# Kernel optimization log

Hardware: AMD Instinct MI355X
Metric: run time of the kernel (lower is better)

Reference implementation:

```python
import jax, jax.numpy as jnp
import numpy as np

N = 50000
E = 1600000
D_IN = 64
D_H = 64
D_EMB = 64
D_DEC = 128
B = 4096


def setup_inputs() -> dict:
    key = jax.random.key(0)
    ks = jax.random.split(key, 16)
    def lin(k, fan_in, fan_out):
        return jax.random.normal(k, (fan_in, fan_out), jnp.float32) / np.sqrt(fan_in)
    inp = {
        "x": jax.random.normal(ks[0], (N, D_IN), jnp.float32),
        "edge_index": jax.random.randint(ks[1], (2, E), 0, N),
        "drug_index": jax.random.randint(ks[2], (B, 2), 1, N),
        "bn_gamma": jnp.ones((D_IN,), jnp.float32),
        "bn_beta": jnp.zeros((D_IN,), jnp.float32),
        "Wu1": lin(ks[3], D_IN, D_H), "Wd1": lin(ks[4], D_IN, D_H), "Wb1": lin(ks[5], D_IN, D_H),
        "Wu2": lin(ks[6], 3 * D_H, D_H), "Wd2": lin(ks[7], 3 * D_H, D_H), "Wb2": lin(ks[8], 3 * D_H, D_H),
        "Wu3": lin(ks[9], 3 * D_H, D_EMB), "Wd3": lin(ks[10], 3 * D_H, D_EMB), "Wb3": lin(ks[11], 3 * D_H, D_EMB),
        "P1": jax.random.normal(ks[12], (3 * D_EMB, D_DEC), jnp.float32),
        "P2": jax.random.normal(ks[13], (D_DEC, D_DEC), jnp.float32),
    }
    return inp


def _batchnorm(x, gamma, beta, eps=1e-5):
    mu = jnp.mean(x, axis=0)
    var = jnp.var(x, axis=0)  # biased, matches torch BN training normalization
    return gamma * (x - mu) / jnp.sqrt(var + eps) + beta


def _bgnn_conv(x, row, col, Wu, Wd, Wb, n_nodes):
    # up direction: messages flow row -> col (source_to_target)
    up = x @ Wu
    dn = x @ Wd
    bi = x @ Wb
    ones = jnp.ones(row.shape[0], x.dtype)
    deg_up = jax.ops.segment_sum(ones, col, num_segments=n_nodes)  # in-degree at col
    x_up = jax.ops.segment_sum(up[row] / deg_up[col][:, None], col, num_segments=n_nodes)
    # down direction: flipped edge_index -> messages flow col -> row
    deg_dn = jax.ops.segment_sum(ones, row, num_segments=n_nodes)
    x_dn = jax.ops.segment_sum(dn[col] / deg_dn[row][:, None], row, num_segments=n_nodes)
    c = jnp.concatenate([x_up, x_dn, bi], axis=-1)
    nrm = jnp.linalg.norm(c, axis=-1, keepdims=True)
    return c / jnp.maximum(nrm, 1e-12)


def _leaky(t):
    return jnp.where(t >= 0, t, 0.1 * t)


def reference(x, edge_index, drug_index, bn_gamma, bn_beta,
              Wu1, Wd1, Wb1, Wu2, Wd2, Wb2, Wu3, Wd3, Wb3, P1, P2):
    row, col = edge_index[0], edge_index[1]
    h = _batchnorm(x, bn_gamma, bn_beta)
    h = _leaky(_bgnn_conv(h, row, col, Wu1, Wd1, Wb1, N))
    h = _leaky(_bgnn_conv(h, row, col, Wu2, Wd2, Wb2, N))
    h = _leaky(_bgnn_conv(h, row, col, Wu3, Wd3, Wb3, N))
    di = jnp.reshape(drug_index, (-1, 2))
    a = h[di[:, 0] - 1]  # [B, 3*D_EMB]
    b = h[di[:, 1] - 1]
    M = P1 @ P2 @ P1.T  # [3*D_EMB, 3*D_EMB]
    ypred = jnp.einsum('bd,de,be->b', a, M, b)[:, None]
    return ypred
```

## Files before the change

kernel.cpp:

```cpp
#include <hip/hip_runtime.h>

#define PN 50000
#define PE 1600000
#define PB 4096
#define NW 8
#define WSZ 6250
#define SCAP 250000
#define NSL 8

typedef __attribute__((ext_vector_type(8))) short bf16x8;
typedef __attribute__((ext_vector_type(4))) float f32x4;

__device__ inline float b2f(ushort u) {
    union { unsigned int i; float f; } x; x.i = ((unsigned int)u) << 16; return x.f;
}
__device__ inline ushort f2b(float f) {
    union { float f; unsigned int i; } x; x.f = f;
    unsigned int r = (x.i + 0x7FFFu + ((x.i >> 16) & 1u)) >> 16;
    return (ushort)r;
}

static constexpr size_t IDXCAP2 = PE + 7 * (size_t)PN + 1024;
static constexpr size_t OFF_BN     = 0;
static constexpr size_t OFF_GCUR   = 256;
static constexpr size_t OFF_TMPM   = 272;
static constexpr size_t OFF_M      = OFF_TMPM + 192 * 128;
static constexpr size_t OFF_DEGU   = OFF_M + 192 * 192;
static constexpr size_t OFF_DEGD   = OFF_DEGU + PN;
static constexpr size_t OFF_OFFU   = OFF_DEGD + PN;
static constexpr size_t OFF_OFFD   = OFF_OFFU + PN + 4;
static constexpr size_t OFF_PHISTU = OFF_OFFD + PN + 4;
static constexpr size_t OFF_PHISTD = OFF_PHISTU + NSL * (size_t)PN;
static constexpr size_t OFF_IDXU   = OFF_PHISTD + NSL * (size_t)PN;
static constexpr size_t OFF_IDXD   = OFF_IDXU + (IDXCAP2 + 1) / 2;
static constexpr size_t OFF_STGU   = OFF_IDXD + (IDXCAP2 + 1) / 2;
static constexpr size_t OFF_STGD   = OFF_STGU + 8 * (size_t)SCAP;
static constexpr size_t OFF_WB16   = OFF_STGD + 8 * (size_t)SCAP;
static constexpr size_t OFF_HB     = OFF_WB16 + 43008;
static constexpr size_t OFF_PROJ   = OFF_HB + (size_t)PN * 96;

__global__ __launch_bounds__(256) void bn_stats_kernel(const float* __restrict__ x,
                                                       float* __restrict__ sums, int N) {
    __shared__ float ls[256], ls2[256];
    int col = threadIdx.x & 63;
    int rstart = blockIdx.x * 4 + (threadIdx.x >> 6);
    float s = 0.f, s2 = 0.f;
    for (int r = rstart; r < N; r += gridDim.x * 4) {
        float v = x[(size_t)r * 64 + col];
        s += v; s2 += v * v;
    }
    ls[threadIdx.x] = s; ls2[threadIdx.x] = s2;
    __syncthreads();
    if (threadIdx.x < 64) {
        s  = ls[threadIdx.x]  + ls[threadIdx.x + 64]  + ls[threadIdx.x + 128]  + ls[threadIdx.x + 192];
        s2 = ls2[threadIdx.x] + ls2[threadIdx.x + 64] + ls2[threadIdx.x + 128] + ls2[threadIdx.x + 192];
        atomicAdd(&sums[col], s);
        atomicAdd(&sums[64 + col], s2);
    }
}

__global__ __launch_bounds__(64) void bn_finalize_kernel(const float* __restrict__ gamma,
                                                         const float* __restrict__ beta,
                                                         float* __restrict__ bn, int N) {
    int c = threadIdx.x;
    float mean = bn[c] / (float)N;
    float var = bn[64 + c] / (float)N - mean * mean;
    float sc = gamma[c] * rsqrtf(var + 1e-5f);
    bn[128 + c] = sc;
    bn[192 + c] = beta[c] - mean * sc;
}

__global__ __launch_bounds__(256) void bin_kernel(const int* __restrict__ ei,
                                                  int* __restrict__ gcur,
                                                  uint* __restrict__ stgu,
                                                  uint* __restrict__ stgd, int E) {
    __shared__ uint sbuf[16][1024];
    __shared__ int scnt[16], sbase[16];
    const int tid = threadIdx.x;
    for (int base = blockIdx.x * 1024; base < E; base += gridDim.x * 1024) {
        if (tid < 16) scnt[tid] = 0;
        __syncthreads();
#pragma unroll
        for (int j = 0; j < 4; ++j) {
            int e = base + j * 256 + tid;
            if (e < E) {
                int r = __builtin_nontemporal_load(&ei[e]);
                int c = __builtin_nontemporal_load(&ei[E + e]);
                int pu = c / WSZ;
                int slot = atomicAdd(&scnt[pu], 1);
                sbuf[pu][slot] = ((uint)c << 16) | (uint)r;
                int pd = r / WSZ;
                int slot2 = atomicAdd(&scnt[8 + pd], 1);
                sbuf[8 + pd][slot2] = ((uint)r << 16) | (uint)c;
            }
        }
        __syncthreads();
        if (tid < 16) sbase[tid] = atomicAdd(&gcur[tid], scnt[tid]);
        __syncthreads();
#pragma unroll 1
        for (int k = 0; k < 16; ++k) {
            int cnt = scnt[k];
            int gb = sbase[k];
            uint* dst = (k < 8) ? (stgu + (size_t)k * SCAP) : (stgd + (size_t)(k - 8) * SCAP);
            for (int i = tid; i < cnt; i += 256) {
                int gi = gb + i;
                if (gi < SCAP) dst[gi] = sbuf[k][i];
            }
        }
        __syncthreads();
    }
}

__global__ __launch_bounds__(256) void hist_kernel(const uint* __restrict__ stgu,
                                                   const uint* __restrict__ stgd,
                                                   const int* __restrict__ gcur,
                                                   int* __restrict__ phistu,
                                                   int* __restrict__ phistd) {
    __shared__ int hist[WSZ];
    const int p = blockIdx.x & 7;
    const int dir = (blockIdx.x >> 3) & 1;
    const int s = blockIdx.x >> 4;
    const int tid = threadIdx.x;
    const int lo = p * WSZ;
    for (int i = tid; i < WSZ; i += 256) hist[i] = 0;
    __syncthreads();
    const int cnt = min(gcur[dir * 8 + p], SCAP);
    const uint* stg = (dir ? stgd : stgu) + (size_t)p * SCAP;
    const int per = (cnt + NSL - 1) / NSL;
    const int s0 = s * per, s1 = min(cnt, s0 + per);
    for (int i = s0 + tid; i < s1; i += 256)
        atomicAdd(&hist[(int)(stg[i] >> 16) - lo], 1);
    __syncthreads();
    int* ph = (dir ? phistd : phistu) + (size_t)s * PN + lo;
    for (int i = tid; i < WSZ; i += 256) ph[i] = hist[i];
}

__global__ __launch_bounds__(1024) void scan_kernel(const int* __restrict__ phA,
                                                    const int* __restrict__ phB,
                                                    int* __restrict__ offA,
                                                    int* __restrict__ offB,
                                                    int* __restrict__ degA,
                                                    int* __restrict__ degB, int len) {
    const int* ph = blockIdx.x ? phB : phA;
    int* off = blockIdx.x ? offB : offA;
    int* dego = blockIdx.x ? degB : degA;
    __shared__ int wsum[17];
    int tid = threadIdx.x, lane = tid & 63, wid = tid >> 6;
    int run = 0;
    for (int base = 0; base < len; base += 4096) {
        int i4 = base + tid * 4;
        int4 v = make_int4(0, 0, 0, 0);
        if (i4 < len) {
#pragma unroll
            for (int sl = 0; sl < NSL; ++sl) {
                int4 t = *(const int4*)&ph[(size_t)sl * len + i4];
                v.x += t.x; v.y += t.y; v.z += t.z; v.w += t.w;
            }
            *(int4*)&dego[i4] = v;
        }
        v.x = (v.x + 7) & ~7; v.y = (v.y + 7) & ~7;
        v.z = (v.z + 7) & ~7; v.w = (v.w + 7) & ~7;
        int lsum = v.x + v.y + v.z + v.w;
        int inc = lsum;
#pragma unroll
        for (int d = 1; d < 64; d <<= 1) {
            int t = __shfl_up(inc, d);
            if (lane >= d) inc += t;
        }
        if (lane == 63) wsum[wid] = inc;
        __syncthreads();
        if (tid == 0) {
            int r2 = 0;
#pragma unroll
            for (int i = 0; i < 16; ++i) { int t = wsum[i]; wsum[i] = r2; r2 += t; }
            wsum[16] = r2;
        }
        __syncthreads();
        if (i4 < len) {
            int pre = run + wsum[wid] + inc - lsum;
            int4 o;
            o.x = pre; o.y = pre + v.x; o.z = o.y + v.y; o.w = o.z + v.z;
            *(int4*)&off[i4] = o;
        }
        run += wsum[16];
        __syncthreads();
    }
    if (tid == 0) off[len] = run;
}

__global__ __launch_bounds__(256) void scatter_kernel(const uint* __restrict__ stgu,
                                                      const uint* __restrict__ stgd,
                                                      const int* __restrict__ gcur,
                                                      const int* __restrict__ phistu,
                                                      const int* __restrict__ phistd,
                                                      const int* __restrict__ offu,
                                                      const int* __restrict__ offd,
                                                      ushort* __restrict__ idxu,
                                                      ushort* __restrict__ idxd) {
    __shared__ int cur[WSZ];
    const int p = blockIdx.x & 7;
    const int dir = (blockIdx.x >> 3) & 1;
    const int s = blockIdx.x >> 4;
    const int tid = threadIdx.x;
    const int lo = p * WSZ;
    const int* off = (dir ? offd : offu);
    const int* phist = (dir ? phistd : phistu);
    for (int i = tid; i < WSZ; i += 256) {
        int c = off[lo + i];
        for (int t = 0; t < s; ++t) c += phist[(size_t)t * PN + lo + i];
        cur[i] = c;
    }
    __syncthreads();
    const int cnt = min(gcur[dir * 8 + p], SCAP);
    const uint* stg = (dir ? stgd : stgu) + (size_t)p * SCAP;
    ushort* idx = (dir ? idxd : idxu);
    const int per = (cnt + NSL - 1) / NSL;
    const int s0 = s * per, s1 = min(cnt, s0 + per);
    for (int i = s0 + tid; i < s1; i += 256) {
        uint u = stg[i];
        int pos = atomicAdd(&cur[(int)(u >> 16) - lo], 1);
        idx[pos] = (ushort)(u & 0xFFFFu);
    }
}

template<int K>
__global__ __launch_bounds__(256) void wconv_kernel(const float* __restrict__ Wu,
                                                    const float* __restrict__ Wd,
                                                    const float* __restrict__ Wb,
                                                    ushort* __restrict__ out) {
    int idx = blockIdx.x * 256 + threadIdx.x;
    if (idx >= 192 * K) return;
    int c = idx / K, k = idx - c * K;
    const float* W = (c < 64) ? Wu : (c < 128 ? Wd : Wb);
    out[idx] = f2b(W[k * 64 + (c & 63)]);
}

template<int K, bool BN>
__global__ __launch_bounds__(256) void gemm_kernel(const ushort* __restrict__ hb,
                                                   const float* __restrict__ x,
                                                   const float* __restrict__ bn,
                                                   const ushort* __restrict__ wb,
                                                   ushort* __restrict__ proj, int nrows) {
    constexpr int KP = K + 8;
    __shared__ ushort wlds[192 * KP];
    const int tid = threadIdx.x;
    constexpr int KB8 = K / 8;
    for (int idx = tid; idx < 192 * KB8; idx += 256) {
        int col = idx / KB8, kb = idx - col * KB8;
        *(bf16x8*)&wlds[col * KP + kb * 8] = *(const bf16x8*)&wb[(size_t)col * K + kb * 8];
    }
    __syncthreads();
    const int lane = tid & 63, wid = tid >> 6;
    const int kgrp = (lane >> 4) * 8;
    const int rbase = blockIdx.x * 128 + wid * 32;
    int ar[2] = { min(rbase + (lane & 15), nrows - 1),
                  min(rbase + 16 + (lane & 15), nrows - 1) };
    f32x4 acc[2][12];
#pragma unroll
    for (int rt = 0; rt < 2; ++rt)
#pragma unroll
        for (int ct = 0; ct < 12; ++ct) acc[rt][ct] = (f32x4)0.0f;

#pragma unroll
    for (int k0 = 0; k0 < K; k0 += 32) {
        bf16x8 af[2];
        if (BN) {
#pragma unroll
            for (int rt = 0; rt < 2; ++rt)
#pragma unroll
                for (int j = 0; j < 8; ++j) {
                    int c = k0 + kgrp + j;
                    float v = x[(size_t)ar[rt] * 64 + c] * bn[128 + c] + bn[192 + c];
                    af[rt][j] = (short)f2b(v);
                }
        } else {
#pragma unroll
            for (int rt = 0; rt < 2; ++rt)
                af[rt] = *(const bf16x8*)&hb[(size_t)ar[rt] * 192 + k0 + kgrp];
        }
#pragma unroll
        for (int ct = 0; ct < 12; ++ct) {
            bf16x8 bfr = *(const bf16x8*)&wlds[(ct * 16 + (lane & 15)) * KP + k0 + kgrp];
            acc[0][ct] = __builtin_amdgcn_mfma_f32_16x16x32_bf16(af[0], bfr, acc[0][ct], 0, 0, 0);
            acc[1][ct] = __builtin_amdgcn_mfma_f32_16x16x32_bf16(af[1], bfr, acc[1][ct], 0, 0, 0);
        }
    }
    const int orow0 = blockIdx.x * 128 + wid * 32 + (lane >> 4) * 4;
#pragma unroll
    for (int rt = 0; rt < 2; ++rt)
#pragma unroll
        for (int ct = 0; ct < 12; ++ct) {
            int ocol = ct * 16 + (lane & 15);
#pragma unroll
            for (int j = 0; j < 4; ++j) {
                int orow = orow0 + rt * 16 + j;
                if (orow < nrows) proj[(size_t)orow * 192 + ocol] = f2b(acc[rt][ct][j]);
            }
        }
}

__global__ __launch_bounds__(256) void gather_kernel(const ushort* __restrict__ proj,
                                                     const int* __restrict__ offu,
                                                     const ushort* __restrict__ idxu,
                                                     const int* __restrict__ degu,
                                                     const int* __restrict__ offd,
                                                     const ushort* __restrict__ idxd,
                                                     const int* __restrict__ degd,
                                                     ushort* __restrict__ hb, int N) {
    int n = blockIdx.x * 4 + (threadIdx.x >> 6);
    if (n >= N) return;
    const int lane = threadIdx.x & 63;
    const int half = lane >> 5;
    const int sl = lane & 31;
    const int du = degu[n], dd = degd[n];
    const int d = half ? dd : du;
    const ushort* __restrict__ pidx = half ? (idxd + offd[n]) : (idxu + offu[n]);
    const uint* __restrict__ rowbase = (const uint*)proj + half * 32 + sl;
    float a0 = 0.f, a1 = 0.f;
    const int dmax = max(du, dd);
    for (int i = 0; i < dmax; i += 4) {
        ushort4 U = *(const ushort4*)(pidx + i);
        int v0 = (i     < d), v1 = (i + 1 < d), v2 = (i + 2 < d), v3 = (i + 3 < d);
        int s0 = v0 ? (int)U.x : 0;
        int s1 = v1 ? (int)U.y : 0;
        int s2 = v2 ? (int)U.z : 0;
        int s3 = v3 ? (int)U.w : 0;
        uint w0 = rowbase[(size_t)s0 * 96];
        uint w1 = rowbase[(size_t)s1 * 96];
        uint w2 = rowbase[(size_t)s2 * 96];
        uint w3 = rowbase[(size_t)s3 * 96];
        if (!v0) w0 = 0; if (!v1) w1 = 0; if (!v2) w2 = 0; if (!v3) w3 = 0;
        a0 += __uint_as_float(w0 << 16) + __uint_as_float(w1 << 16)
            + __uint_as_float(w2 << 16) + __uint_as_float(w3 << 16);
        a1 += __uint_as_float(w0 & 0xFFFF0000u) + __uint_as_float(w1 & 0xFFFF0000u)
            + __uint_as_float(w2 & 0xFFFF0000u) + __uint_as_float(w3 & 0xFFFF0000u);
    }
    float scale = 1.0f / (float)max(d, 1);
    a0 *= scale; a1 *= scale;
    uint bw = (half == 0) ? ((const uint*)proj)[(size_t)n * 96 + 64 + sl] : 0u;
    float b0 = __uint_as_float(bw << 16);
    float b1 = __uint_as_float(bw & 0xFFFF0000u);
    float ss = a0 * a0 + a1 * a1 + b0 * b0 + b1 * b1;
#pragma unroll
    for (int off = 32; off; off >>= 1) ss += __shfl_xor(ss, off);
    float r = 1.0f / fmaxf(sqrtf(ss), 1e-12f);
    a0 *= r; a1 *= r; b0 *= r; b1 *= r;
    a0 = a0 >= 0.f ? a0 : 0.1f * a0;
    a1 = a1 >= 0.f ? a1 : 0.1f * a1;
    uint* hb32 = (uint*)hb;
    hb32[(size_t)n * 96 + half * 32 + sl] = (uint)f2b(a0) | ((uint)f2b(a1) << 16);
    if (half == 0) {
        b0 = b0 >= 0.f ? b0 : 0.1f * b0;
        b1 = b1 >= 0.f ? b1 : 0.1f * b1;
        hb32[(size_t)n * 96 + 64 + sl] = (uint)f2b(b0) | ((uint)f2b(b1) << 16);
    }
}

__global__ __launch_bounds__(128) void m1_kernel(const float* __restrict__ P1,
                                                 const float* __restrict__ P2,
                                                 float* __restrict__ tmpM) {
    int i = blockIdx.x, c = threadIdx.x;
    float s = 0.f;
    for (int k = 0; k < 128; ++k) s += P1[i * 128 + k] * P2[k * 128 + c];
    tmpM[i * 128 + c] = s;
}

__global__ __launch_bounds__(192) void m2_kernel(const float* __restrict__ tmpM,
                                                 const float* __restrict__ P1,
                                                 float* __restrict__ M) {
    __shared__ float trow[128];
    int i = blockIdx.x, j = threadIdx.x;
    if (j < 128) trow[j] = tmpM[i * 128 + j];
    __syncthreads();
    float s = 0.f;
    for (int k = 0; k < 128; ++k) s += trow[k] * P1[j * 128 + k];
    M[i * 192 + j] = s;
}

__global__ __launch_bounds__(192) void decode_kernel(const ushort* __restrict__ hb,
                                                     const int* __restrict__ di,
                                                     const float* __restrict__ M,
                                                     float* __restrict__ out) {
    __shared__ alignas(16) float bvs[8][192];
    __shared__ float red[3][8];
    int pb = blockIdx.x * 8;
    int i = threadIdx.x;
#pragma unroll
    for (int p = 0; p < 8; ++p) {
        int nb = di[(pb + p) * 2 + 1] - 1;
        bvs[p][i] = b2f(hb[(size_t)nb * 192 + i]);
    }
    __syncthreads();
    float t[8] = {};
    const float4* M4 = (const float4*)(M + (size_t)i * 192);
    for (int j4 = 0; j4 < 48; ++j4) {
        float4 m = M4[j4];
#pragma unroll
        for (int p = 0; p < 8; ++p) {
            float4 b = *(const float4*)&bvs[p][j4 * 4];
            t[p] += m.x * b.x + m.y * b.y + m.z * b.z + m.w * b.w;
        }
    }
    int wid = i >> 6, lane = i & 63;
#pragma unroll
    for (int p = 0; p < 8; ++p) {
        int na = di[(pb + p) * 2] - 1;
        float v = b2f(hb[(size_t)na * 192 + i]) * t[p];
#pragma unroll
        for (int off = 32; off; off >>= 1) v += __shfl_xor(v, off);
        if (lane == 0) red[wid][p] = v;
    }
    __syncthreads();
    if (i < 8) out[pb + i] = red[0][i] + red[1][i] + red[2][i];
}

extern "C" void kernel_launch(void* const* d_in, const int* in_sizes, int n_in,
                              void* d_out, int out_size, void* d_ws, size_t ws_size,
                              hipStream_t stream) {
    const float* x     = (const float*)d_in[0];
    const int*   ei    = (const int*)d_in[1];
    const int*   di    = (const int*)d_in[2];
    const float* gamma = (const float*)d_in[3];
    const float* beta  = (const float*)d_in[4];
    const float* Wu[3] = {(const float*)d_in[5], (const float*)d_in[8],  (const float*)d_in[11]};
    const float* Wd[3] = {(const float*)d_in[6], (const float*)d_in[9],  (const float*)d_in[12]};
    const float* Wb[3] = {(const float*)d_in[7], (const float*)d_in[10], (const float*)d_in[13]};
    const float* P1    = (const float*)d_in[14];
    const float* P2    = (const float*)d_in[15];
    float* out = (float*)d_out;
    float* ws  = (float*)d_ws;

    float* bn    = ws + OFF_BN;
    int* gcur  = (int*)(ws + OFF_GCUR);
    float* tmpM  = ws + OFF_TMPM;
    float* M     = ws + OFF_M;
    int* degu  = (int*)(ws + OFF_DEGU);
    int* degd  = (int*)(ws + OFF_DEGD);
    int* offu  = (int*)(ws + OFF_OFFU);
    int* offd  = (int*)(ws + OFF_OFFD);
    int* phistu = (int*)(ws + OFF_PHISTU);
    int* phistd = (int*)(ws + OFF_PHISTD);
    ushort* idxu = (ushort*)(ws + OFF_IDXU);
    ushort* idxd = (ushort*)(ws + OFF_IDXD);
    uint* stgu = (uint*)(ws + OFF_STGU);
    uint* stgd = (uint*)(ws + OFF_STGD);
    ushort* wb16 = (ushort*)(ws + OFF_WB16);
    ushort* hb   = (ushort*)(ws + OFF_HB);
    ushort* proj = (ushort*)(ws + OFF_PROJ);
    ushort* wbl[3] = {wb16, wb16 + 12288, wb16 + 49152};

    hipMemsetAsync(ws, 0, 272 * sizeof(float), stream);

    bn_stats_kernel<<<200, 256, 0, stream>>>(x, bn, PN);
    bn_finalize_kernel<<<1, 64, 0, stream>>>(gamma, beta, bn, PN);

    bin_kernel<<<512, 256, 0, stream>>>(ei, gcur, stgu, stgd, PE);
    hist_kernel<<<16 * NSL, 256, 0, stream>>>(stgu, stgd, gcur, phistu, phistd);
    scan_kernel<<<2, 1024, 0, stream>>>(phistu, phistd, offu, offd, degu, degd, PN);
    scatter_kernel<<<16 * NSL, 256, 0, stream>>>(stgu, stgd, gcur, phistu, phistd,
                                                 offu, offd, idxu, idxd);

    wconv_kernel<64><<<(192 * 64 + 255) / 256, 256, 0, stream>>>(Wu[0], Wd[0], Wb[0], wbl[0]);
    wconv_kernel<192><<<(192 * 192 + 255) / 256, 256, 0, stream>>>(Wu[1], Wd[1], Wb[1], wbl[1]);
    wconv_kernel<192><<<(192 * 192 + 255) / 256, 256, 0, stream>>>(Wu[2], Wd[2], Wb[2], wbl[2]);

    const int ngb = (PN + 127) / 128;
    gemm_kernel<64, true><<<ngb, 256, 0, stream>>>(hb, x, bn, wbl[0], proj, PN);
    gather_kernel<<<(PN + 3) / 4, 256, 0, stream>>>(proj, offu, idxu, degu, offd, idxd, degd, hb, PN);
    gemm_kernel<192, false><<<ngb, 256, 0, stream>>>(hb, x, bn, wbl[1], proj, PN);
    gather_kernel<<<(PN + 3) / 4, 256, 0, stream>>>(proj, offu, idxu, degu, offd, idxd, degd, hb, PN);
    gemm_kernel<192, false><<<ngb, 256, 0, stream>>>(hb, x, bn, wbl[2], proj, PN);
    gather_kernel<<<(PN + 3) / 4, 256, 0, stream>>>(proj, offu, idxu, degu, offd, idxd, degd, hb, PN);

    m1_kernel<<<192, 128, 0, stream>>>(P1, P2, tmpM);
    m2_kernel<<<192, 192, 0, stream>>>(tmpM, P1, M);
    decode_kernel<<<PB / 8, 192, 0, stream>>>(hb, di, M, out);
}
```

Measured before the change: 637.1 us.

## Sub-bucket CSR edges by source window and gather window-by-window across nodes

```diff
diff --git a/kernel.cpp b/kernel.cpp
--- a/kernel.cpp
+++ b/kernel.cpp
@@ -3,10 +3,14 @@
 #define PN 50000
 #define PE 1600000
 #define PB 4096
-#define NW 8
-#define WSZ 6250
-#define SCAP 250000
-#define NSL 8
+#define NP 8
+#define PSZ 6250
+#define NSW 4
+#define SWSZ 12500
+#define SCAP 210000
+#define NSL 4
+#define GBLK 2048
+#define NPER 7
 
 typedef __attribute__((ext_vector_type(8))) short bf16x8;
 typedef __attribute__((ext_vector_type(4))) float f32x4;
@@ -20,22 +24,23 @@
     return (ushort)r;
 }
 
-static constexpr size_t IDXCAP2 = PE + 7 * (size_t)PN + 1024;
+static constexpr size_t L4N = 4 * (size_t)PN;
+static constexpr size_t IDXCAP3 = PE + 3 * L4N + 1024;
 static constexpr size_t OFF_BN     = 0;
 static constexpr size_t OFF_GCUR   = 256;
 static constexpr size_t OFF_TMPM   = 272;
 static constexpr size_t OFF_M      = OFF_TMPM + 192 * 128;
-static constexpr size_t OFF_DEGU   = OFF_M + 192 * 192;
-static constexpr size_t OFF_DEGD   = OFF_DEGU + PN;
-static constexpr size_t OFF_OFFU   = OFF_DEGD + PN;
-static constexpr size_t OFF_OFFD   = OFF_OFFU + PN + 4;
-static constexpr size_t OFF_PHISTU = OFF_OFFD + PN + 4;
-static constexpr size_t OFF_PHISTD = OFF_PHISTU + NSL * (size_t)PN;
-static constexpr size_t OFF_IDXU   = OFF_PHISTD + NSL * (size_t)PN;
-static constexpr size_t OFF_IDXD   = OFF_IDXU + (IDXCAP2 + 1) / 2;
-static constexpr size_t OFF_STGU   = OFF_IDXD + (IDXCAP2 + 1) / 2;
-static constexpr size_t OFF_STGD   = OFF_STGU + 8 * (size_t)SCAP;
-static constexpr size_t OFF_WB16   = OFF_STGD + 8 * (size_t)SCAP;
+static constexpr size_t OFF_WOFFU  = OFF_M + 192 * 192;
+static constexpr size_t OFF_WOFFD  = OFF_WOFFU + L4N + 4;
+static constexpr size_t OFF_WDEGU  = OFF_WOFFD + L4N + 4;
+static constexpr size_t OFF_WDEGD  = OFF_WDEGU + L4N;
+static constexpr size_t OFF_PHISTU = OFF_WDEGD + L4N;
+static constexpr size_t OFF_PHISTD = OFF_PHISTU + NSL * L4N;
+static constexpr size_t OFF_IDXU   = OFF_PHISTD + NSL * L4N;
+static constexpr size_t OFF_IDXD   = OFF_IDXU + (IDXCAP3 + 1) / 2;
+static constexpr size_t OFF_STGU   = OFF_IDXD + (IDXCAP3 + 1) / 2;
+static constexpr size_t OFF_STGD   = OFF_STGU + NP * (size_t)SCAP;
+static constexpr size_t OFF_WB16   = OFF_STGD + NP * (size_t)SCAP;
 static constexpr size_t OFF_HB     = OFF_WB16 + 43008;
 static constexpr size_t OFF_PROJ   = OFF_HB + (size_t)PN * 96;
 
@@ -86,10 +91,10 @@
             if (e < E) {
                 int r = __builtin_nontemporal_load(&ei[e]);
                 int c = __builtin_nontemporal_load(&ei[E + e]);
-                int pu = c / WSZ;
+                int pu = c / PSZ;
                 int slot = atomicAdd(&scnt[pu], 1);
                 sbuf[pu][slot] = ((uint)c << 16) | (uint)r;
-                int pd = r / WSZ;
+                int pd = r / PSZ;
                 int slot2 = atomicAdd(&scnt[8 + pd], 1);
                 sbuf[8 + pd][slot2] = ((uint)r << 16) | (uint)c;
             }
@@ -116,23 +121,27 @@
                                                    const int* __restrict__ gcur,
                                                    int* __restrict__ phistu,
                                                    int* __restrict__ phistd) {
-    __shared__ int hist[WSZ];
+    __shared__ int hist[PSZ * NSW];
     const int p = blockIdx.x & 7;
     const int dir = (blockIdx.x >> 3) & 1;
     const int s = blockIdx.x >> 4;
     const int tid = threadIdx.x;
-    const int lo = p * WSZ;
-    for (int i = tid; i < WSZ; i += 256) hist[i] = 0;
+    const int lo = p * PSZ;
+    for (int i = tid; i < PSZ * NSW; i += 256) hist[i] = 0;
     __syncthreads();
     const int cnt = min(gcur[dir * 8 + p], SCAP);
     const uint* stg = (dir ? stgd : stgu) + (size_t)p * SCAP;
     const int per = (cnt + NSL - 1) / NSL;
     const int s0 = s * per, s1 = min(cnt, s0 + per);
-    for (int i = s0 + tid; i < s1; i += 256)
-        atomicAdd(&hist[(int)(stg[i] >> 16) - lo], 1);
-    __syncthreads();
-    int* ph = (dir ? phistd : phistu) + (size_t)s * PN + lo;
-    for (int i = tid; i < WSZ; i += 256) ph[i] = hist[i];
+    for (int i = s0 + tid; i < s1; i += 256) {
+        uint u = stg[i];
+        int ld = (int)(u >> 16) - lo;
+        int w = (int)(u & 0xFFFFu) / SWSZ;
+        atomicAdd(&hist[ld * NSW + w], 1);
+    }
+    __syncthreads();
+    int* ph = (dir ? phistd : phistu) + (size_t)s * L4N + (size_t)lo * NSW;
+    for (int i = tid; i < PSZ * NSW; i += 256) ph[i] = hist[i];
 }
 
 __global__ __launch_bounds__(1024) void scan_kernel(const int* __restrict__ phA,
@@ -158,8 +167,8 @@
             }
             *(int4*)&dego[i4] = v;
         }
-        v.x = (v.x + 7) & ~7; v.y = (v.y + 7) & ~7;
-        v.z = (v.z + 7) & ~7; v.w = (v.w + 7) & ~7;
+        v.x = (v.x + 3) & ~3; v.y = (v.y + 3) & ~3;
+        v.z = (v.z + 3) & ~3; v.w = (v.w + 3) & ~3;
         int lsum = v.x + v.y + v.z + v.w;
         int inc = lsum;
 #pragma unroll
@@ -193,21 +202,22 @@
                                                       const int* __restrict__ gcur,
                                                       const int* __restrict__ phistu,
                                                       const int* __restrict__ phistd,
-                                                      const int* __restrict__ offu,
-                                                      const int* __restrict__ offd,
+                                                      const int* __restrict__ woffu,
+                                                      const int* __restrict__ woffd,
                                                       ushort* __restrict__ idxu,
                                                       ushort* __restrict__ idxd) {
-    __shared__ int cur[WSZ];
+    __shared__ int cur[PSZ * NSW];
     const int p = blockIdx.x & 7;
     const int dir = (blockIdx.x >> 3) & 1;
     const int s = blockIdx.x >> 4;
     const int tid = threadIdx.x;
-    const int lo = p * WSZ;
-    const int* off = (dir ? offd : offu);
+    const int lo = p * PSZ;
+    const int* off = (dir ? woffd : woffu);
     const int* phist = (dir ? phistd : phistu);
-    for (int i = tid; i < WSZ; i += 256) {
-        int c = off[lo + i];
-        for (int t = 0; t < s; ++t) c += phist[(size_t)t * PN + lo + i];
+    const size_t gb = (size_t)lo * NSW;
+    for (int i = tid; i < PSZ * NSW; i += 256) {
+        int c = off[gb + i];
+        for (int t = 0; t < s; ++t) c += phist[(size_t)t * L4N + gb + i];
         cur[i] = c;
     }
     __syncthreads();
@@ -218,8 +228,10 @@
     const int s0 = s * per, s1 = min(cnt, s0 + per);
     for (int i = s0 + tid; i < s1; i += 256) {
         uint u = stg[i];
-        int pos = atomicAdd(&cur[(int)(u >> 16) - lo], 1);
-        idx[pos] = (ushort)(u & 0xFFFFu);
+        int src = (int)(u & 0xFFFFu);
+        int li = ((int)(u >> 16) - lo) * NSW + src / SWSZ;
+        int pos = atomicAdd(&cur[li], 1);
+        idx[pos] = (ushort)src;
     }
 }
 
@@ -300,59 +312,83 @@
 }
 
 __global__ __launch_bounds__(256) void gather_kernel(const ushort* __restrict__ proj,
-                                                     const int* __restrict__ offu,
+                                                     const int* __restrict__ woffu,
+                                                     const int* __restrict__ wdegu,
+                                                     const int* __restrict__ woffd,
+                                                     const int* __restrict__ wdegd,
                                                      const ushort* __restrict__ idxu,
-                                                     const int* __restrict__ degu,
-                                                     const int* __restrict__ offd,
                                                      const ushort* __restrict__ idxd,
-                                                     const int* __restrict__ degd,
                                                      ushort* __restrict__ hb, int N) {
-    int n = blockIdx.x * 4 + (threadIdx.x >> 6);
-    if (n >= N) return;
+    const int gw = blockIdx.x * 4 + (threadIdx.x >> 6);
+    const int nwaves = gridDim.x * 4;
     const int lane = threadIdx.x & 63;
     const int half = lane >> 5;
     const int sl = lane & 31;
-    const int du = degu[n], dd = degd[n];
-    const int d = half ? dd : du;
-    const ushort* __restrict__ pidx = half ? (idxd + offd[n]) : (idxu + offu[n]);
-    const uint* __restrict__ rowbase = (const uint*)proj + half * 32 + sl;
-    float a0 = 0.f, a1 = 0.f;
-    const int dmax = max(du, dd);
-    for (int i = 0; i < dmax; i += 4) {
-        ushort4 U = *(const ushort4*)(pidx + i);
-        int v0 = (i     < d), v1 = (i + 1 < d), v2 = (i + 2 < d), v3 = (i + 3 < d);
-        int s0 = v0 ? (int)U.x : 0;
-        int s1 = v1 ? (int)U.y : 0;
-        int s2 = v2 ? (int)U.z : 0;
-        int s3 = v3 ? (int)U.w : 0;
-        uint w0 = rowbase[(size_t)s0 * 96];
-        uint w1 = rowbase[(size_t)s1 * 96];
-        uint w2 = rowbase[(size_t)s2 * 96];
-        uint w3 = rowbase[(size_t)s3 * 96];
-        if (!v0) w0 = 0; if (!v1) w1 = 0; if (!v2) w2 = 0; if (!v3) w3 = 0;
-        a0 += __uint_as_float(w0 << 16) + __uint_as_float(w1 << 16)
-            + __uint_as_float(w2 << 16) + __uint_as_float(w3 << 16);
-        a1 += __uint_as_float(w0 & 0xFFFF0000u) + __uint_as_float(w1 & 0xFFFF0000u)
-            + __uint_as_float(w2 & 0xFFFF0000u) + __uint_as_float(w3 & 0xFFFF0000u);
-    }
-    float scale = 1.0f / (float)max(d, 1);
-    a0 *= scale; a1 *= scale;
-    uint bw = (half == 0) ? ((const uint*)proj)[(size_t)n * 96 + 64 + sl] : 0u;
-    float b0 = __uint_as_float(bw << 16);
-    float b1 = __uint_as_float(bw & 0xFFFF0000u);
-    float ss = a0 * a0 + a1 * a1 + b0 * b0 + b1 * b1;
-#pragma unroll
-    for (int off = 32; off; off >>= 1) ss += __shfl_xor(ss, off);
-    float r = 1.0f / fmaxf(sqrtf(ss), 1e-12f);
-    a0 *= r; a1 *= r; b0 *= r; b1 *= r;
-    a0 = a0 >= 0.f ? a0 : 0.1f * a0;
-    a1 = a1 >= 0.f ? a1 : 0.1f * a1;
+    const int* __restrict__ woff = half ? woffd : woffu;
+    const int* __restrict__ wdeg = half ? wdegd : wdegu;
+    const ushort* __restrict__ idx = half ? idxd : idxu;
+    const uint* __restrict__ rowb = (const uint*)proj + half * 32 + sl;
+
+    float a0[NPER], a1[NPER];
+    int dtot[NPER];
+#pragma unroll
+    for (int j = 0; j < NPER; ++j) { a0[j] = 0.f; a1[j] = 0.f; dtot[j] = 0; }
+
+    for (int w = 0; w < NSW; ++w) {
+#pragma unroll
+        for (int j = 0; j < NPER; ++j) {
+            int n = gw + j * nwaves;
+            if (n < N) {
+                int key = n * NSW + w;
+                int s = woff[key];
+                int cnt = wdeg[key];
+                dtot[j] += cnt;
+                const ushort* p = idx + s;
+                for (int i = 0; i < cnt; i += 4) {
+                    ushort4 U = *(const ushort4*)(p + i);
+                    int v1 = (i + 1 < cnt), v2 = (i + 2 < cnt), v3 = (i + 3 < cnt);
+                    int s0 = (int)U.x;
+                    int s1 = v1 ? (int)U.y : 0;
+                    int s2 = v2 ? (int)U.z : 0;
+                    int s3 = v3 ? (int)U.w : 0;
+                    uint w0 = rowb[(size_t)s0 * 96];
+                    uint w1 = rowb[(size_t)s1 * 96];
+                    uint w2 = rowb[(size_t)s2 * 96];
+                    uint w3 = rowb[(size_t)s3 * 96];
+                    if (!v1) w1 = 0; if (!v2) w2 = 0; if (!v3) w3 = 0;
+                    a0[j] += __uint_as_float(w0 << 16) + __uint_as_float(w1 << 16)
+                           + __uint_as_float(w2 << 16) + __uint_as_float(w3 << 16);
+                    a1[j] += __uint_as_float(w0 & 0xFFFF0000u) + __uint_as_float(w1 & 0xFFFF0000u)
+                           + __uint_as_float(w2 & 0xFFFF0000u) + __uint_as_float(w3 & 0xFFFF0000u);
+                }
+            }
+        }
+        __syncthreads();
+    }
+
     uint* hb32 = (uint*)hb;
-    hb32[(size_t)n * 96 + half * 32 + sl] = (uint)f2b(a0) | ((uint)f2b(a1) << 16);
-    if (half == 0) {
-        b0 = b0 >= 0.f ? b0 : 0.1f * b0;
-        b1 = b1 >= 0.f ? b1 : 0.1f * b1;
-        hb32[(size_t)n * 96 + 64 + sl] = (uint)f2b(b0) | ((uint)f2b(b1) << 16);
+#pragma unroll
+    for (int j = 0; j < NPER; ++j) {
+        int n = gw + j * nwaves;
+        if (n >= N) continue;
+        float sc = 1.0f / (float)max(dtot[j], 1);
+        float A0 = a0[j] * sc, A1 = a1[j] * sc;
+        uint bw = (half == 0) ? ((const uint*)proj)[(size_t)n * 96 + 64 + sl] : 0u;
+        float b0 = __uint_as_float(bw << 16);
+        float b1 = __uint_as_float(bw & 0xFFFF0000u);
+        float ss = A0 * A0 + A1 * A1 + b0 * b0 + b1 * b1;
+#pragma unroll
+        for (int off = 32; off; off >>= 1) ss += __shfl_xor(ss, off);
+        float r = 1.0f / fmaxf(sqrtf(ss), 1e-12f);
+        A0 *= r; A1 *= r; b0 *= r; b1 *= r;
+        A0 = A0 >= 0.f ? A0 : 0.1f * A0;
+        A1 = A1 >= 0.f ? A1 : 0.1f * A1;
+        hb32[(size_t)n * 96 + half * 32 + sl] = (uint)f2b(A0) | ((uint)f2b(A1) << 16);
+        if (half == 0) {
+            b0 = b0 >= 0.f ? b0 : 0.1f * b0;
+            b1 = b1 >= 0.f ? b1 : 0.1f * b1;
+            hb32[(size_t)n * 96 + 64 + sl] = (uint)f2b(b0) | ((uint)f2b(b1) << 16);
+        }
     }
 }
 
@@ -434,10 +470,10 @@
     int* gcur  = (int*)(ws + OFF_GCUR);
     float* tmpM  = ws + OFF_TMPM;
     float* M     = ws + OFF_M;
-    int* degu  = (int*)(ws + OFF_DEGU);
-    int* degd  = (int*)(ws + OFF_DEGD);
-    int* offu  = (int*)(ws + OFF_OFFU);
-    int* offd  = (int*)(ws + OFF_OFFD);
+    int* woffu = (int*)(ws + OFF_WOFFU);
+    int* woffd = (int*)(ws + OFF_WOFFD);
+    int* wdegu = (int*)(ws + OFF_WDEGU);
+    int* wdegd = (int*)(ws + OFF_WDEGD);
     int* phistu = (int*)(ws + OFF_PHISTU);
     int* phistd = (int*)(ws + OFF_PHISTD);
     ushort* idxu = (ushort*)(ws + OFF_IDXU);
@@ -456,9 +492,9 @@
 
     bin_kernel<<<512, 256, 0, stream>>>(ei, gcur, stgu, stgd, PE);
     hist_kernel<<<16 * NSL, 256, 0, stream>>>(stgu, stgd, gcur, phistu, phistd);
-    scan_kernel<<<2, 1024, 0, stream>>>(phistu, phistd, offu, offd, degu, degd, PN);
+    scan_kernel<<<2, 1024, 0, stream>>>(phistu, phistd, woffu, woffd, wdegu, wdegd, (int)L4N);
     scatter_kernel<<<16 * NSL, 256, 0, stream>>>(stgu, stgd, gcur, phistu, phistd,
-                                                 offu, offd, idxu, idxd);
+                                                 woffu, woffd, idxu, idxd);
 
     wconv_kernel<64><<<(192 * 64 + 255) / 256, 256, 0, stream>>>(Wu[0], Wd[0], Wb[0], wbl[0]);
     wconv_kernel<192><<<(192 * 192 + 255) / 256, 256, 0, stream>>>(Wu[1], Wd[1], Wb[1], wbl[1]);
@@ -466,11 +502,11 @@
 
     const int ngb = (PN + 127) / 128;
     gemm_kernel<64, true><<<ngb, 256, 0, stream>>>(hb, x, bn, wbl[0], proj, PN);
-    gather_kernel<<<(PN + 3) / 4, 256, 0, stream>>>(proj, offu, idxu, degu, offd, idxd, degd, hb, PN);
+    gather_kernel<<<GBLK, 256, 0, stream>>>(proj, woffu, wdegu, woffd, wdegd, idxu, idxd, hb, PN);
     gemm_kernel<192, false><<<ngb, 256, 0, stream>>>(hb, x, bn, wbl[1], proj, PN);
-    gather_kernel<<<(PN + 3) / 4, 256, 0, stream>>>(proj, offu, idxu, degu, offd, idxd, degd, hb, PN);
+    gather_kernel<<<GBLK, 256, 0, stream>>>(proj, woffu, wdegu, woffd, wdegd, idxu, idxd, hb, PN);
     gemm_kernel<192, false><<<ngb, 256, 0, stream>>>(hb, x, bn, wbl[2], proj, PN);
-    gather_kernel<<<(PN + 3) / 4, 256, 0, stream>>>(proj, offu, idxu, degu, offd, idxd, degd, hb, PN);
+    gather_kernel<<<GBLK, 256, 0, stream>>>(proj, woffu, wdegu, woffd, wdegd, idxu, idxd, hb, PN);
 
     m1_kernel<<<192, 128, 0, stream>>>(P1, P2, tmpM);
     m2_kernel<<<192, 192, 0, stream>>>(tmpM, P1, M);
```

Result: slower. 752.3 us (+18.1%).
